# Performance work log

Measured on AMD Instinct MI355X. Metric: run time of the kernel, lower is better.

Reference implementation:

```python
import jax, jax.numpy as jnp
import numpy as np

N = 100000
E = 1600000
IN_DIM = 1024
H_DIM = 16
DIM2 = H_DIM * 8  # 128


def _xavier(key, shape):
    fan_in, fan_out = shape[-2], shape[-1]
    lim = (6.0 / (fan_in + fan_out)) ** 0.5
    return jax.random.uniform(key, shape, jnp.float32, -lim, lim)


def setup_inputs() -> dict:
    key = jax.random.key(0)
    ks = jax.random.split(key, 10)
    x = jax.random.normal(ks[0], (N, IN_DIM), jnp.float32)
    edge_index = jax.random.randint(ks[1], (2, E), 0, N)
    perm = jax.random.permutation(ks[2], N)
    W1 = _xavier(ks[3], (IN_DIM, DIM2)); b1 = jnp.zeros((DIM2,), jnp.float32)
    W2 = _xavier(ks[4], (DIM2, DIM2)); b2 = jnp.zeros((DIM2,), jnp.float32)
    W3 = _xavier(ks[5], (DIM2, H_DIM)); b3 = jnp.zeros((H_DIM,), jnp.float32)
    Wdo = _xavier(ks[6], (1, DIM2, DIM2)); bdo = jnp.zeros((1,), jnp.float32)
    Wdh = _xavier(ks[7], (1, H_DIM, H_DIM)); bdh = jnp.zeros((1,), jnp.float32)
    return dict(x=x, W1=W1, b1=b1, W2=W2, b2=b2, W3=W3, b3=b3,
                Wdo=Wdo, bdo=bdo, Wdh=Wdh, bdh=bdh,
                edge_index=edge_index, perm=perm)


def _graph_conv(x, W, b, src, dst, norm_src, norm_dst):
    # DGL GraphConv, norm='both': D_dst^{-1/2} A D_src^{-1/2} X W + b
    h = (x * norm_src[:, None]) @ W          # mult W first (in >= out)
    agg = jax.ops.segment_sum(h[src], dst, num_segments=N)
    return agg * norm_dst[:, None] + b


def _l2norm(x):
    n = jnp.sqrt(jnp.sum(x * x, axis=1, keepdims=True))
    return x / jnp.maximum(n, 1e-12)


def _bilinear(a, c, W, b):
    # nn.Bilinear(n_h, n_h, 1): out[n,k] = a[n] @ W[k] @ c[n] + b[k]
    return jnp.einsum('nd,kde,ne->nk', a, W, c) + b


def reference(x, W1, b1, W2, b2, W3, b3, Wdo, bdo, Wdh, bdh, edge_index, perm):
    src, dst = edge_index[0], edge_index[1]
    ones = jnp.ones((E,), jnp.float32)
    deg_out = jnp.maximum(jax.ops.segment_sum(ones, src, num_segments=N), 1.0)
    deg_in = jnp.maximum(jax.ops.segment_sum(ones, dst, num_segments=N), 1.0)
    ns, nd = deg_out ** -0.5, deg_in ** -0.5

    def encode(xin):
        o = _graph_conv(xin, W1, b1, src, dst, ns, nd)
        o = _graph_conv(o, W2, b2, src, dst, ns, nd) + o
        h = _graph_conv(o, W3, b3, src, dst, ns, nd)
        emb_o = jax.nn.relu(o)
        g_o = jax.nn.sigmoid(_l2norm(emb_o))
        emb_h = jax.nn.relu(h)
        g_h = jax.nn.sigmoid(_l2norm(emb_h))
        return h, emb_o, g_o, emb_h, g_h

    h, emb_o, g_o, emb_h, g_h = encode(x)
    h_a, emb_oa, g_oa, emb_ha, g_ha = encode(x[perm])

    def disc(c, h_pl, h_mi, W, b):
        return jnp.concatenate([_bilinear(h_pl, c, W, b), _bilinear(h_mi, c, W, b)], axis=1)

    ret_o = disc(g_o, emb_o, emb_oa, Wdo, bdo)
    ret_oa = disc(g_oa, emb_oa, emb_o, Wdo, bdo)
    ret_h = disc(g_h, emb_h, emb_ha, Wdh, bdh)
    ret_ha = disc(g_ha, emb_ha, emb_h, Wdh, bdh)
    return (h, ret_o, ret_h, ret_oa, ret_ha)
```

## Files before the change

### kernel.cpp

```cpp
#include <hip/hip_runtime.h>
#include <math.h>

#define NN 100000
#define EE 1600000
#define SCB 98
#define GB1 782
#define FB 3125

typedef __attribute__((ext_vector_type(8))) short bf16x8;
typedef __attribute__((ext_vector_type(4))) short bf16x4;
typedef __attribute__((ext_vector_type(4))) float f32x4;

__device__ __forceinline__ unsigned short f2bf(float x){
  union { float f; unsigned u; } v; v.f = x;
  unsigned r = v.u + 0x7FFFu + ((v.u >> 16) & 1u);
  return (unsigned short)(r >> 16);
}
__device__ __forceinline__ float bf2f(unsigned short h){
  union { unsigned u; float f; } v; v.u = ((unsigned)h) << 16; return v.f;
}
__device__ __forceinline__ float sigm(float x){ return 1.0f/(1.0f+__expf(-x)); }

__device__ __forceinline__ void barrier_lds_only(){
  asm volatile("s_waitcnt lgkmcnt(0)" ::: "memory");
  __builtin_amdgcn_s_barrier();
  __builtin_amdgcn_sched_barrier(0);
}

__global__ __launch_bounds__(256) void k_deg_wcvt(const int* __restrict__ src, const int* __restrict__ dst,
                      int* __restrict__ dout, int* __restrict__ din,
                      const float* __restrict__ W1, const float* __restrict__ W2,
                      const float* __restrict__ Wdo, const float* __restrict__ W3,
                      unsigned short* __restrict__ W1T, unsigned short* __restrict__ W2T,
                      unsigned short* __restrict__ WdoB, unsigned short* __restrict__ W3c){
  int b = blockIdx.x;
  if (b < EE/256){
    int e = b*256 + threadIdx.x;
    atomicAdd(&dout[src[e]],1); atomicAdd(&din[dst[e]],1);
  } else {
    int i = (b - EE/256)*256 + threadIdx.x;
    if (i < 131072){
      int c = i>>13, r = i&8191, col = r>>6, k = c*64 + (r&63);
      W1T[i] = f2bf(W1[(size_t)k*128 + col]);
    } else if (i < 147456){
      int j = i-131072;
      int c = j>>13, r = j&8191, col = r>>6, k = c*64 + (r&63);
      W2T[j] = f2bf(W2[(size_t)k*128 + col]);
    } else if (i < 163840){
      int j = i-147456;
      int c = j>>13, r = j&8191, col = r>>6, k = c*64 + (r&63);
      WdoB[j] = f2bf(Wdo[(size_t)col*128 + k]);
    } else if (i < 165888){
      int j = i-163840;
      int col = j>>7, k = j&127;
      W3c[j] = f2bf(W3[(size_t)k*16 + col]);
    }
  }
}

__global__ __launch_bounds__(1024) void k_scan1(const int* __restrict__ din, int* __restrict__ chunk,
                        int* __restrict__ bsum){
  __shared__ int wsum[16];
  int t = threadIdx.x, lane = t & 63, w = t >> 6;
  int i = blockIdx.x*1024 + t;
  int v = (i < NN) ? din[i] : 0;
  int x = v;
  #pragma unroll
  for (int off=1; off<64; off<<=1){
    int y = __shfl_up(x, off);
    if (lane>=off) x += y;
  }
  if (lane==63) wsum[w] = x;
  __syncthreads();
  int pre = 0;
  #pragma unroll
  for (int j=0;j<16;j++) if (j<w) pre += wsum[j];
  int incl = x + pre;
  if (i < NN) chunk[i] = incl;
  if (t == 1023) bsum[blockIdx.x] = incl;
}

__global__ __launch_bounds__(128) void k_scan2(const int* __restrict__ bsum, int* __restrict__ bpre,
                       int* __restrict__ row_ptr){
  __shared__ int w0tot;
  int t = threadIdx.x, lane = t & 63, w = t >> 6;
  int v = (t < SCB) ? bsum[t] : 0;
  int x = v;
  #pragma unroll
  for (int off=1; off<64; off<<=1){
    int y = __shfl_up(x, off);
    if (lane>=off) x += y;
  }
  if (w==0 && lane==63) w0tot = x;
  __syncthreads();
  int incl = x + (w ? w0tot : 0);
  if (t < SCB) bpre[t] = incl - v;
  if (t == 0) row_ptr[0] = 0;
}

__global__ __launch_bounds__(256) void k_scan3(const int* __restrict__ din, const int* __restrict__ chunk,
                       const int* __restrict__ bpre, const int* __restrict__ dout,
                       const int* __restrict__ perm,
                       int* __restrict__ row_ptr, int* __restrict__ cursor,
                       float* __restrict__ ns, float* __restrict__ nd, int* __restrict__ inv){
  int i = blockIdx.x*256 + threadIdx.x;
  if (i < NN){
    int d = din[i];
    int val = chunk[i] + bpre[i>>10];
    row_ptr[i+1] = val;
    cursor[i] = val - d;
    ns[i] = rsqrtf((float)max(dout[i],1));
    nd[i] = rsqrtf((float)max(d,1));
    inv[perm[i]] = i;
  }
}

__global__ __launch_bounds__(512,4) void k_g1fill(
    const float* __restrict__ A, const unsigned short* __restrict__ Wc,
    unsigned short* __restrict__ z, const float* __restrict__ ns,
    const int* __restrict__ inv,
    const int* __restrict__ src, const int* __restrict__ dst,
    int* __restrict__ cursor, int* __restrict__ col)
{
  constexpr int NC = 16;
  __shared__ __align__(16) unsigned short As[2*128*72];
  __shared__ __align__(16) unsigned short Bs[2*128*64];
  if (blockIdx.x >= GB1){
    int e = (blockIdx.x - GB1)*512 + threadIdx.x;
    if (e < EE){
      int pos = atomicAdd(&cursor[dst[e]],1);
      col[pos] = src[e];
    }
    return;
  }
  int t = threadIdx.x, wave = t>>6, lane = t&63;
  int row0 = blockIdx.x*128;

  int srow = t>>4;
  int scol4 = (t&15)*4;
  int colB = t>>2;
  int s0B = (t&3)*2;

  f32x4 acc[8] = {};
  float4 S0[4], S1[4];
  bf16x8 w0{}, w1{};

#define ALOAD(SET, CC) { \
  _Pragma("unroll") \
  for (int p=0;p<4;p++){ \
    int rr = min(row0 + p*32 + srow, NN-1); \
    SET[p] = *(const float4*)(A + (size_t)rr*1024 + (CC)*64 + scol4); } }

#define AWRITE(SET, BUF) { \
  _Pragma("unroll") \
  for (int p=0;p<4;p++){ \
    short4 s4; \
    s4.x = (short)f2bf(SET[p].x); s4.y = (short)f2bf(SET[p].y); \
    s4.z = (short)f2bf(SET[p].z); s4.w = (short)f2bf(SET[p].w); \
    *(short4*)&As[(BUF)*9216 + (p*32+srow)*72 + scol4] = s4; } }

#define BLOAD(CC) { \
  const unsigned short* gp = Wc + (size_t)(CC)*8192 + (size_t)t*16; \
  w0 = *(const bf16x8*)(gp); \
  w1 = *(const bf16x8*)(gp+8); }

#define BWRITE(BUF) { \
  unsigned short* bb = &Bs[(BUF)*8192]; \
  *(bf16x8*)&bb[colB*64 + ((s0B     ^ (colB&7))<<3)] = w0; \
  *(bf16x8*)&bb[colB*64 + (((s0B+1) ^ (colB&7))<<3)] = w1; }

  ALOAD(S0, 0);
  BLOAD(0);
  AWRITE(S0, 0);
  BWRITE(0);
  ALOAD(S1, 1);
  BLOAD(1);
  barrier_lds_only();

  int slot0 = lane>>4;
  int c = lane & 15;
  int arow = wave*16 + (lane&15);
  #pragma unroll
  for (int cc=0; cc<NC; ++cc){
    if (cc+2 < NC){
      if (cc&1) { ALOAD(S1, cc+2); } else { ALOAD(S0, cc+2); }
    }
    int cur = cc&1;
    const unsigned short* ab = &As[cur*9216];
    const unsigned short* bb = &Bs[cur*8192];
    {
      bf16x8 af = *(const bf16x8*)&ab[arow*72 + (slot0<<3)];
      #pragma unroll
      for (int j=0;j<8;j++){
        int cj = j*16 + c;
        bf16x8 b = *(const bf16x8*)&bb[cj*64 + ((slot0 ^ (cj&7))<<3)];
        acc[j] = __builtin_amdgcn_mfma_f32_16x16x32_bf16(af, b, acc[j], 0, 0, 0);
      }
    }
    {
      bf16x8 af = *(const bf16x8*)&ab[arow*72 + 32 + (slot0<<3)];
      #pragma unroll
      for (int j=0;j<8;j++){
        int cj = j*16 + c;
        bf16x8 b = *(const bf16x8*)&bb[cj*64 + (((slot0+4) ^ (cj&7))<<3)];
        acc[j] = __builtin_amdgcn_mfma_f32_16x16x32_bf16(af, b, acc[j], 0, 0, 0);
      }
    }
    if (cc+1 < NC){
      int nb = (cc+1)&1;
      if (cc&1) { AWRITE(S0, nb); } else { AWRITE(S1, nb); }
      BWRITE(nb);
      barrier_lds_only();
      if (cc+2 < NC) BLOAD(cc+2);
    }
  }
#undef ALOAD
#undef AWRITE
#undef BLOAD
#undef BWRITE

  int rbase = row0 + wave*16 + (lane>>4)*4;
  #pragma unroll
  for (int j=0;j<8;j++){
    int colx = j*16 + c;
    #pragma unroll
    for (int r=0;r<4;r++){
      int row = rbase + r;
      if (row < NN){
        float v = acc[j][r];
        z[(size_t)row*256 + colx] = f2bf(v * ns[row]);
        int ir = inv[row];
        z[(size_t)ir*256 + 128 + colx] = f2bf(v * ns[ir]);
      }
    }
  }
}

struct ARU { bf16x8 a; };
__device__ __forceinline__ void aload(ARU& r, const unsigned short* p){
  r.a = *(const bf16x8*)p;
}
template<int IM>
__device__ __forceinline__ bf16x8 aconv(const ARU& r, float rs){
  if constexpr (IM==0) return r.a;
  else {
    bf16x8 o;
    #pragma unroll
    for (int i=0;i<8;i++){
      float v = sigm(fmaxf(bf2f((unsigned short)r.a[i]),0.0f)*rs);
      o[i] = (short)f2bf(v);
    }
    return o;
  }
}
__device__ __forceinline__ bf16x8 araw(const ARU& r){ return r.a; }

template<int KDIM, int IN_MODE, int OUT_MODE>
__global__ __launch_bounds__(256,2) void k_gemmA(
    const unsigned short* __restrict__ A, const unsigned short* __restrict__ Wc,
    unsigned short* __restrict__ out0,
    const float* __restrict__ scale,
    const float* __restrict__ rn, int nrows,
    float* __restrict__ ro, float* __restrict__ roa,
    const unsigned short* __restrict__ W3c, const float* __restrict__ ns2,
    unsigned short* __restrict__ th)
{
  constexpr int NC = KDIM/64;
  __shared__ __align__(16) unsigned short Bs[2*128*64];
  __shared__ __align__(16) unsigned short W3s[OUT_MODE==3 ? 16*128 : 16];
  int t = threadIdx.x, wave = t>>6, lane = t&63;
  int row0 = blockIdx.x*64;
  int arow = row0 + wave*16 + (lane&15);
  int kof = (lane>>4)*8;
  int arow_c = min(arow, nrows-1);
  const unsigned short* ap = A + (size_t)arow_c*KDIM + kof;
  float rscale = 1.0f;
  if constexpr (IN_MODE==1) rscale = rn[arow_c];

  int scol = t>>3;
  int sw = ((t&7) ^ (scol&7))<<3;

  unsigned short* b0 = &Bs[0];
  unsigned short* b1 = &Bs[128*64];
  const unsigned short* bcur = b0; unsigned short* bnxt = b1;

  f32x4 acc[8] = {};
  f32x4 acc2 = {};
  ARU A0a{},A0b{},A1a{},A1b{},A2a{},A2b{};
  bf16x8 w0{},w1{},w2{},w3{};

  {
    const unsigned short* gp = Wc + (size_t)t*8;
    bf16x8 t0 = *(const bf16x8*)(gp);
    bf16x8 t1 = *(const bf16x8*)(gp+2048);
    bf16x8 t2 = *(const bf16x8*)(gp+4096);
    bf16x8 t3 = *(const bf16x8*)(gp+6144);
    *(bf16x8*)&b0[(0*32+scol)*64 + sw] = t0;
    *(bf16x8*)&b0[(1*32+scol)*64 + sw] = t1;
    *(bf16x8*)&b0[(2*32+scol)*64 + sw] = t2;
    *(bf16x8*)&b0[(3*32+scol)*64 + sw] = t3;
  }
  if constexpr (OUT_MODE==3){
    int wc = t>>4, wsl = t&15;
    bf16x8 v = *(const bf16x8*)(W3c + wc*128 + wsl*8);
    *(bf16x8*)&W3s[wc*128 + ((wsl ^ (wc&7))<<3)] = v;
  }
  aload(A0a, ap); aload(A0b, ap+32);
  if (NC>1){
    const unsigned short* gp = Wc + 8192 + (size_t)t*8;
    w0 = *(const bf16x8*)(gp);
    w1 = *(const bf16x8*)(gp+2048);
    w2 = *(const bf16x8*)(gp+4096);
    w3 = *(const bf16x8*)(gp+6144);
    aload(A1a, ap+64); aload(A1b, ap+96);
  }
  __syncthreads();

  int slot0 = lane>>4;
  int c = lane & 15;
  #pragma unroll
  for (int cc=0; cc<NC; ++cc){
    if (cc+2 < NC){
      aload(A2a, ap + (cc+2)*64);
      aload(A2b, ap + (cc+2)*64 + 32);
    }
    {
      bf16x8 af = aconv<IN_MODE>(A0a, rscale);
      #pragma unroll
      for (int j=0;j<8;j++){
        int cj = j*16 + c;
        bf16x8 b = *(const bf16x8*)&bcur[cj*64 + ((slot0 ^ (cj&7))<<3)];
        acc[j] = __builtin_amdgcn_mfma_f32_16x16x32_bf16(af, b, acc[j], 0, 0, 0);
      }
      if constexpr (OUT_MODE==3){
        int sl = cc*8 + slot0;
        bf16x8 b = *(const bf16x8*)&W3s[c*128 + ((sl ^ (c&7))<<3)];
        acc2 = __builtin_amdgcn_mfma_f32_16x16x32_bf16(araw(A0a), b, acc2, 0, 0, 0);
      }
    }
    {
      bf16x8 af = aconv<IN_MODE>(A0b, rscale);
      #pragma unroll
      for (int j=0;j<8;j++){
        int cj = j*16 + c;
        bf16x8 b = *(const bf16x8*)&bcur[cj*64 + (((slot0+4) ^ (cj&7))<<3)];
        acc[j] = __builtin_amdgcn_mfma_f32_16x16x32_bf16(af, b, acc[j], 0, 0, 0);
      }
      if constexpr (OUT_MODE==3){
        int sl = cc*8 + 4 + slot0;
        bf16x8 b = *(const bf16x8*)&W3s[c*128 + ((sl ^ (c&7))<<3)];
        acc2 = __builtin_amdgcn_mfma_f32_16x16x32_bf16(araw(A0b), b, acc2, 0, 0, 0);
      }
    }
    if (cc+1 < NC){
      *(bf16x8*)&bnxt[(0*32+scol)*64 + sw] = w0;
      *(bf16x8*)&bnxt[(1*32+scol)*64 + sw] = w1;
      *(bf16x8*)&bnxt[(2*32+scol)*64 + sw] = w2;
      *(bf16x8*)&bnxt[(3*32+scol)*64 + sw] = w3;
      barrier_lds_only();
      const unsigned short* tmp = bcur; bcur = bnxt; bnxt = (unsigned short*)tmp;
      if (cc+2 < NC){
        const unsigned short* gp = Wc + (size_t)(cc+2)*8192 + (size_t)t*8;
        w0 = *(const bf16x8*)(gp);
        w1 = *(const bf16x8*)(gp+2048);
        w2 = *(const bf16x8*)(gp+4096);
        w3 = *(const bf16x8*)(gp+6144);
      }
    }
    A0a=A1a; A0b=A1b; A1a=A2a; A1b=A2b;
  }

  if constexpr (OUT_MODE==3){
    #pragma unroll
    for (int r=0;r<4;r++){
      int row = row0 + wave*16 + (lane>>4)*4 + r;
      int sidx = row>=NN ? row-NN : row;
      float v = acc2[r]*ns2[sidx];
      size_t tof = row<NN ? (size_t)row*32 + c : (size_t)(row-NN)*32 + 16 + c;
      th[tof] = f2bf(v);
    }
    __syncthreads();
    unsigned short* Os = &Bs[0];
    unsigned short* Oo = &Bs[8192];
    for (int p=t; p<2048; p+=256){
      int r = (p>>4)&63, seg = p&15;
      int row = row0 + r;
      int srcrow = (p<1024) ? row : (row<NN ? row+NN : row-NN);
      unsigned short* dst = (p<1024) ? Os : Oo;
      *(bf16x8*)&dst[r*128 + ((seg ^ (r&7))<<3)] = *(const bf16x8*)&A[(size_t)srcrow*128 + seg*8];
    }
    __syncthreads();
    float bb = scale[0];
    #pragma unroll
    for (int r=0;r<4;r++){
      int lr = wave*16 + (lane>>4)*4 + r;
      float dsame=0.f, doth=0.f;
      #pragma unroll
      for (int j=0;j<8;j++){
        float v = acc[j][r];
        int colj = j*16 + c;
        int idx = lr*128 + (((colj>>3) ^ (lr&7))<<3) + (colj&7);
        dsame += fmaxf(bf2f(Os[idx]),0.f)*v;
        doth  += fmaxf(bf2f(Oo[idx]),0.f)*v;
      }
      #pragma unroll
      for (int off=1; off<16; off<<=1){
        dsame += __shfl_xor(dsame, off);
        doth  += __shfl_xor(doth, off);
      }
      if (c==0){
        int row = row0 + lr;
        if (row < NN){
          ro[(size_t)row*2+0] = dsame + bb;
          ro[(size_t)row*2+1] = doth + bb;
        } else {
          int m = row - NN;
          roa[(size_t)m*2+0] = dsame + bb;
          roa[(size_t)m*2+1] = doth + bb;
        }
      }
    }
  } else {
    int rbase = row0 + wave*16 + (lane>>4)*4;
    #pragma unroll
    for (int j=0;j<8;j++){
      int colx = j*16 + c;
      #pragma unroll
      for (int r=0;r<4;r++){
        int row = rbase + r;
        if (row < nrows){
          float v = acc[j][r];
          int sidx = row >= NN ? row - NN : row;
          size_t zof = row < NN ? (size_t)row*256 + colx : (size_t)(row-NN)*256 + 128 + colx;
          out0[zof] = f2bf(v * scale[sidx]);
        }
      }
    }
  }
}

template<bool RESID>
__global__ __launch_bounds__(256) void k_agg128(
  const unsigned short* __restrict__ z,
  const int* __restrict__ row_ptr, const int* __restrict__ col,
  const float* __restrict__ nd, const float* __restrict__ bias,
  unsigned short* __restrict__ ob, float* __restrict__ rn)
{
  int wave = threadIdx.x>>6, lane = threadIdx.x&63;
  int row = blockIdx.x*4 + wave;
  if (row >= NN) return;
  int s = row_ptr[row], e = row_ptr[row+1];
  int es = lane>>5;
  int half = (lane>>4)&1;
  int c8 = (lane&15)*8;
  size_t lof = (size_t)half*128 + c8;
  float acc[8] = {};
  int i = s + es;
  int c0 = (i   < e) ? col[i]   : -1;
  int c1 = (i+2 < e) ? col[i+2] : -1;
  int c2 = (i+4 < e) ? col[i+4] : -1;
  int c3 = (i+6 < e) ? col[i+6] : -1;
  bf16x8 u0 = {}, u1 = {}, u2 = {}, u3 = {};
  if (c0 >= 0) u0 = *(const bf16x8*)(z + (size_t)c0*256 + lof);
  if (c1 >= 0) u1 = *(const bf16x8*)(z + (size_t)c1*256 + lof);
  if (c2 >= 0) u2 = *(const bf16x8*)(z + (size_t)c2*256 + lof);
  if (c3 >= 0) u3 = *(const bf16x8*)(z + (size_t)c3*256 + lof);
  while (c0 >= 0){
    int n0 = (i+8  < e) ? col[i+8]  : -1;
    int n1 = (i+10 < e) ? col[i+10] : -1;
    bf16x8 w0 = {}, w1 = {};
    if (n0 >= 0) w0 = *(const bf16x8*)(z + (size_t)n0*256 + lof);
    if (n1 >= 0) w1 = *(const bf16x8*)(z + (size_t)n1*256 + lof);
    #pragma unroll
    for (int j=0;j<8;j++) acc[j] += bf2f((unsigned short)u0[j]) + bf2f((unsigned short)u1[j]);
    c0 = c2; c1 = c3; u0 = u2; u1 = u3;
    c2 = n0; c3 = n1; u2 = w0; u3 = w1;
    i += 4;
  }
  #pragma unroll
  for (int j=0;j<8;j++) acc[j] += __shfl_down(acc[j], 32);
  if (lane < 32){
    float ndr = nd[row];
    size_t oof = half ? (size_t)(NN+row)*128 + c8 : (size_t)row*128 + c8;
    float ra[8];
    #pragma unroll
    for (int j=0;j<8;j++) ra[j] = acc[j]*ndr + bias[c8+j];
    if constexpr (RESID){
      bf16x8 pv = *(const bf16x8*)(ob + oof);
      #pragma unroll
      for (int j=0;j<8;j++) ra[j] += bf2f((unsigned short)pv[j]);
    }
    bf16x8 wv;
    #pragma unroll
    for (int j=0;j<8;j++) wv[j] = (short)f2bf(ra[j]);
    *(bf16x8*)(ob + oof) = wv;
    if constexpr (RESID){
      float sa = 0.f;
      #pragma unroll
      for (int j=0;j<8;j++){ float x1 = fmaxf(ra[j],0.f); sa += x1*x1; }
      sa += __shfl_down(sa, 8);
      sa += __shfl_down(sa, 4);
      sa += __shfl_down(sa, 2);
      sa += __shfl_down(sa, 1);
      if ((lane&15)==0) rn[half ? NN+row : row] = 1.0f/fmaxf(sqrtf(sa),1e-12f);
    }
  }
}

__global__ __launch_bounds__(256) void k_agg16(
  const unsigned short* __restrict__ th,
  const int* __restrict__ row_ptr, const int* __restrict__ col,
  const float* __restrict__ nd, const float* __restrict__ b3,
  const float* __restrict__ Wdh, const float* __restrict__ bdh,
  float* __restrict__ hout, float* __restrict__ rh, float* __restrict__ rha)
{
  __shared__ float Ws[256];
  __shared__ float hbuf[4][32];
  __shared__ float gbuf[4][32];
  int t = threadIdx.x;
  Ws[t] = Wdh[t];
  __syncthreads();
  int wave = t>>6, lane = t&63;
  int row = blockIdx.x*4 + wave;
  if (row >= NN) return;
  int s = row_ptr[row], e = row_ptr[row+1];
  int es = lane>>3, l8 = lane&7;
  float a4[4] = {};
  int i = s + es;
  int c0 = (i   <e)? col[i]    : -1;
  int c1 = (i+8 <e)? col[i+8]  : -1;
  int c2 = (i+16<e)? col[i+16] : -1;
  int c3 = (i+24<e)? col[i+24] : -1;
  bf16x4 u0 = {}, u1 = {}, u2 = {}, u3 = {};
  if (c0 >= 0) u0 = *(const bf16x4*)(th + (size_t)c0*32 + l8*4);
  if (c1 >= 0) u1 = *(const bf16x4*)(th + (size_t)c1*32 + l8*4);
  if (c2 >= 0) u2 = *(const bf16x4*)(th + (size_t)c2*32 + l8*4);
  if (c3 >= 0) u3 = *(const bf16x4*)(th + (size_t)c3*32 + l8*4);
  while (c0 >= 0){
    int n0 = (i+32<e)? col[i+32] : -1;
    int n1 = (i+40<e)? col[i+40] : -1;
    bf16x4 w0 = {}, w1 = {};
    if (n0 >= 0) w0 = *(const bf16x4*)(th + (size_t)n0*32 + l8*4);
    if (n1 >= 0) w1 = *(const bf16x4*)(th + (size_t)n1*32 + l8*4);
    #pragma unroll
    for (int j=0;j<4;j++) a4[j] += bf2f((unsigned short)u0[j]) + bf2f((unsigned short)u1[j]);
    c0 = c2; c1 = c3; u0 = u2; u1 = u3;
    c2 = n0; c3 = n1; u2 = w0; u3 = w1;
    i += 16;
  }
  #pragma unroll
  for (int j=0;j<4;j++){
    a4[j] += __shfl_down(a4[j], 32);
    a4[j] += __shfl_down(a4[j], 16);
    a4[j] += __shfl_down(a4[j], 8);
  }
  if (lane < 8){
    float ndr = nd[row];
    int half = l8>>2, c0x = (l8&3)*4;
    float4 r;
    r.x = a4[0]*ndr + b3[c0x+0];
    r.y = a4[1]*ndr + b3[c0x+1];
    r.z = a4[2]*ndr + b3[c0x+2];
    r.w = a4[3]*ndr + b3[c0x+3];
    if (half==0) *(float4*)&hout[(size_t)row*16 + c0x] = r;
    int hb = half*16 + c0x;
    hbuf[wave][hb+0]=r.x; hbuf[wave][hb+1]=r.y; hbuf[wave][hb+2]=r.z; hbuf[wave][hb+3]=r.w;
  }
  if (lane < 16){
    int d = lane;
    float e1v = fmaxf(hbuf[wave][d],    0.f);
    float e2v = fmaxf(hbuf[wave][16+d], 0.f);
    float s1 = e1v*e1v, s2 = e2v*e2v;
    #pragma unroll
    for (int off=1; off<16; off<<=1){
      s1 += __shfl_xor(s1, off);
      s2 += __shfl_xor(s2, off);
    }
    float r1 = 1.0f/fmaxf(sqrtf(s1),1e-12f);
    float r2 = 1.0f/fmaxf(sqrtf(s2),1e-12f);
    gbuf[wave][d]    = sigm(e1v*r1);
    gbuf[wave][16+d] = sigm(e2v*r2);
    float vh1=0.f, vh2=0.f;
    #pragma unroll
    for (int e2i=0;e2i<16;e2i++){
      float w = Ws[d*16+e2i];
      vh1 += w*gbuf[wave][e2i];
      vh2 += w*gbuf[wave][16+e2i];
    }
    float q00 = e1v*vh1, q01 = e2v*vh1, q10 = e2v*vh2, q11 = e1v*vh2;
    #pragma unroll
    for (int off=1; off<16; off<<=1){
      q00 += __shfl_xor(q00, off);
      q01 += __shfl_xor(q01, off);
      q10 += __shfl_xor(q10, off);
      q11 += __shfl_xor(q11, off);
    }
    if (lane==0){
      float bb = bdh[0];
      rh [(size_t)row*2+0]=q00+bb; rh [(size_t)row*2+1]=q01+bb;
      rha[(size_t)row*2+0]=q10+bb; rha[(size_t)row*2+1]=q11+bb;
    }
  }
}

extern "C" void kernel_launch(void* const* d_in, const int* in_sizes, int n_in,
                              void* d_out, int out_size, void* d_ws, size_t ws_size,
                              hipStream_t stream){
  const float* x   = (const float*)d_in[0];
  const float* W1  = (const float*)d_in[1];
  const float* b1  = (const float*)d_in[2];
  const float* W2  = (const float*)d_in[3];
  const float* b2  = (const float*)d_in[4];
  const float* W3  = (const float*)d_in[5];
  const float* b3  = (const float*)d_in[6];
  const float* Wdo = (const float*)d_in[7];
  const float* bdo = (const float*)d_in[8];
  const float* Wdh = (const float*)d_in[9];
  const float* bdh = (const float*)d_in[10];
  const int* ei    = (const int*)d_in[11];
  const int* perm  = (const int*)d_in[12];
  const int* esrc = ei;
  const int* edst = ei + EE;

  char* ws = (char*)d_ws;
  size_t off = 0;
  auto alloc = [&](size_t bytes)->void*{ void* p = ws + off; off += (bytes + 255) & ~(size_t)255; return p; };
  unsigned short* z  = (unsigned short*)alloc((size_t)NN*256*2);
  unsigned short* ob = (unsigned short*)alloc((size_t)2*NN*128*2);
  unsigned short* th = (unsigned short*)alloc((size_t)NN*32*2);
  int* deg = (int*)alloc((size_t)2*NN*4);
  int* dout_ = deg; int* din_ = deg + NN;
  float* ns = (float*)alloc((size_t)NN*4);
  float* nd = (float*)alloc((size_t)NN*4);
  int* inv  = (int*)alloc((size_t)NN*4);
  float* rn = (float*)alloc((size_t)2*NN*4);
  int* cursor = (int*)alloc((size_t)NN*4);
  int* row_ptr = (int*)alloc((size_t)(NN+1)*4);
  int* colx = (int*)alloc((size_t)EE*4);
  int* chunk = (int*)alloc((size_t)NN*4);
  int* bsum = (int*)alloc((size_t)SCB*4);
  int* bpre = (int*)alloc((size_t)SCB*4);
  unsigned short* W1T = (unsigned short*)alloc((size_t)1024*128*2);
  unsigned short* W2T = (unsigned short*)alloc((size_t)128*128*2);
  unsigned short* WdoB = (unsigned short*)alloc((size_t)128*128*2);
  unsigned short* W3c = (unsigned short*)alloc((size_t)16*128*2);

  float* out_h   = (float*)d_out;
  float* out_ro  = out_h  + (size_t)NN*16;
  float* out_rh  = out_ro + (size_t)NN*2;
  float* out_roa = out_rh + (size_t)NN*2;
  float* out_rha = out_roa+ (size_t)NN*2;

  hipMemsetAsync(deg, 0, (size_t)2*NN*4, stream);
  k_deg_wcvt<<<EE/256 + 648, 256, 0, stream>>>(esrc, edst, dout_, din_,
                                               W1, W2, Wdo, W3, W1T, W2T, WdoB, W3c);
  k_scan1<<<SCB, 1024, 0, stream>>>(din_, chunk, bsum);
  k_scan2<<<1, 128, 0, stream>>>(bsum, bpre, row_ptr);
  k_scan3<<<(NN+255)/256, 256, 0, stream>>>(din_, chunk, bpre, dout_, perm, row_ptr, cursor, ns, nd, inv);

  int gb2 = (2*NN)/64;
  k_g1fill<<<GB1 + FB, 512, 0, stream>>>(x, W1T, z, ns, inv, esrc, edst, cursor, colx);
  k_agg128<false><<<(NN+3)/4,256,0,stream>>>(z, row_ptr, colx, nd, b1, ob, nullptr);
  k_gemmA<128,0,1><<<gb2,256,0,stream>>>(ob, W2T, z, ns, nullptr, 2*NN,
                                         nullptr, nullptr, nullptr, nullptr, nullptr);
  k_agg128<true><<<(NN+3)/4,256,0,stream>>>(z, row_ptr, colx, nd, b2, ob, rn);
  k_gemmA<128,1,3><<<gb2,256,0,stream>>>(ob, WdoB, nullptr, bdo, rn, 2*NN,
                                         out_ro, out_roa, W3c, ns, th);
  k_agg16<<<(NN+3)/4,256,0,stream>>>(th, row_ptr, colx, nd, b3, Wdh, bdh, out_h, out_rh, out_rha);
}
```

Measured before the change: 683.5 us.

## Store unscaled layer-1 product once and apply perm and norm during aggregation

The first GEMM now writes a single unscaled bf16 128-wide product per node instead of writing both the scaled original row and the scaled permuted copy into a 256-wide buffer. A new aggregation kernel reads the source row directly (through perm for the augmented half) and multiplies by ns[src] per edge, so the GEMM epilogue no longer performs scattered writes via inv. This halves the GEMM output traffic and removes the random scatter. In exchange, the aggregation does extra perm and ns gathers per edge, and its permuted-half reads become less regular.

```diff
diff --git a/kernel.cpp b/kernel.cpp
--- a/kernel.cpp
+++ b/kernel.cpp
@@ -117,8 +117,7 @@
 
 __global__ __launch_bounds__(512,4) void k_g1fill(
     const float* __restrict__ A, const unsigned short* __restrict__ Wc,
-    unsigned short* __restrict__ z, const float* __restrict__ ns,
-    const int* __restrict__ inv,
+    unsigned short* __restrict__ tz,
     const int* __restrict__ src, const int* __restrict__ dst,
     int* __restrict__ cursor, int* __restrict__ col)
 {
@@ -226,13 +225,64 @@
     #pragma unroll
     for (int r=0;r<4;r++){
       int row = rbase + r;
-      if (row < NN){
-        float v = acc[j][r];
-        z[(size_t)row*256 + colx] = f2bf(v * ns[row]);
-        int ir = inv[row];
-        z[(size_t)ir*256 + 128 + colx] = f2bf(v * ns[ir]);
-      }
-    }
+      if (row < NN) tz[(size_t)row*128 + colx] = f2bf(acc[j][r]);
+    }
+  }
+}
+
+__global__ __launch_bounds__(256) void k_agg1(
+  const unsigned short* __restrict__ tz, const int* __restrict__ perm,
+  const float* __restrict__ ns,
+  const int* __restrict__ row_ptr, const int* __restrict__ col,
+  const float* __restrict__ nd, const float* __restrict__ bias,
+  unsigned short* __restrict__ ob)
+{
+  int wave = threadIdx.x>>6, lane = threadIdx.x&63;
+  int row = blockIdx.x*4 + wave;
+  if (row >= NN) return;
+  int s = row_ptr[row], e = row_ptr[row+1];
+  int es = lane>>5;
+  int half = (lane>>4)&1;
+  int c8 = (lane&15)*8;
+  float acc[8] = {};
+  bf16x8 zer = {};
+  int i = s + es;
+
+#define FETCH1(IDX, U, F) { \
+  if ((IDX) < e){ \
+    int sc = col[(IDX)]; \
+    int rr = half ? perm[sc] : sc; \
+    F = ns[sc]; \
+    U = *(const bf16x8*)(tz + (size_t)rr*128 + c8); \
+  } else { F = 0.0f; U = zer; } }
+
+  bf16x8 u0, u1, u2, u3;
+  float f0, f1, f2, f3;
+  FETCH1(i,   u0, f0);
+  FETCH1(i+2, u1, f1);
+  FETCH1(i+4, u2, f2);
+  FETCH1(i+6, u3, f3);
+  while (i < e){
+    bf16x8 w0, w1; float g0, g1;
+    FETCH1(i+8,  w0, g0);
+    FETCH1(i+10, w1, g1);
+    #pragma unroll
+    for (int j=0;j<8;j++)
+      acc[j] += bf2f((unsigned short)u0[j])*f0 + bf2f((unsigned short)u1[j])*f1;
+    u0=u2; f0=f2; u1=u3; f1=f3;
+    u2=w0; f2=g0; u3=w1; f3=g1;
+    i += 4;
+  }
+#undef FETCH1
+  #pragma unroll
+  for (int j=0;j<8;j++) acc[j] += __shfl_down(acc[j], 32);
+  if (lane < 32){
+    float ndr = nd[row];
+    size_t oof = half ? (size_t)(NN+row)*128 + c8 : (size_t)row*128 + c8;
+    bf16x8 wv;
+    #pragma unroll
+    for (int j=0;j<8;j++) wv[j] = (short)f2bf(acc[j]*ndr + bias[c8+j]);
+    *(bf16x8*)(ob + oof) = wv;
   }
 }
 
@@ -439,7 +489,6 @@
   }
 }
 
-template<bool RESID>
 __global__ __launch_bounds__(256) void k_agg128(
   const unsigned short* __restrict__ z,
   const int* __restrict__ row_ptr, const int* __restrict__ col,
@@ -485,7 +534,7 @@
     float ra[8];
     #pragma unroll
     for (int j=0;j<8;j++) ra[j] = acc[j]*ndr + bias[c8+j];
-    if constexpr (RESID){
+    {
       bf16x8 pv = *(const bf16x8*)(ob + oof);
       #pragma unroll
       for (int j=0;j<8;j++) ra[j] += bf2f((unsigned short)pv[j]);
@@ -494,7 +543,7 @@
     #pragma unroll
     for (int j=0;j<8;j++) wv[j] = (short)f2bf(ra[j]);
     *(bf16x8*)(ob + oof) = wv;
-    if constexpr (RESID){
+    {
       float sa = 0.f;
       #pragma unroll
       for (int j=0;j<8;j++){ float x1 = fmaxf(ra[j],0.f); sa += x1*x1; }
@@ -627,6 +676,7 @@
   auto alloc = [&](size_t bytes)->void*{ void* p = ws + off; off += (bytes + 255) & ~(size_t)255; return p; };
   unsigned short* z  = (unsigned short*)alloc((size_t)NN*256*2);
   unsigned short* ob = (unsigned short*)alloc((size_t)2*NN*128*2);
+  unsigned short* tz = (unsigned short*)alloc((size_t)NN*128*2);
   unsigned short* th = (unsigned short*)alloc((size_t)NN*32*2);
   int* deg = (int*)alloc((size_t)2*NN*4);
   int* dout_ = deg; int* din_ = deg + NN;
@@ -659,11 +709,11 @@
   k_scan3<<<(NN+255)/256, 256, 0, stream>>>(din_, chunk, bpre, dout_, perm, row_ptr, cursor, ns, nd, inv);
 
   int gb2 = (2*NN)/64;
-  k_g1fill<<<GB1 + FB, 512, 0, stream>>>(x, W1T, z, ns, inv, esrc, edst, cursor, colx);
-  k_agg128<false><<<(NN+3)/4,256,0,stream>>>(z, row_ptr, colx, nd, b1, ob, nullptr);
+  k_g1fill<<<GB1 + FB, 512, 0, stream>>>(x, W1T, tz, esrc, edst, cursor, colx);
+  k_agg1<<<(NN+3)/4,256,0,stream>>>(tz, perm, ns, row_ptr, colx, nd, b1, ob);
   k_gemmA<128,0,1><<<gb2,256,0,stream>>>(ob, W2T, z, ns, nullptr, 2*NN,
                                          nullptr, nullptr, nullptr, nullptr, nullptr);
-  k_agg128<true><<<(NN+3)/4,256,0,stream>>>(z, row_ptr, colx, nd, b2, ob, rn);
+  k_agg128<<<(NN+3)/4,256,0,stream>>>(z, row_ptr, colx, nd, b2, ob, rn);
   k_gemmA<128,1,3><<<gb2,256,0,stream>>>(ob, WdoB, nullptr, bdo, rn, 2*NN,
                                          out_ro, out_roa, W3c, ns, th);
   k_agg16<<<(NN+3)/4,256,0,stream>>>(th, row_ptr, colx, nd, b3, Wdh, bdh, out_h, out_rh, out_rha);
```

New measurement: 699.1 us. 2.3% more time.
